# Optimization experiments

Measured on AMD Instinct MI355X. Metric: run time of the kernel, lower is better.

The kernel has to match this reference:

```python
import jax, jax.numpy as jnp
import numpy as np

N = 50000   # nodes
E = 400000  # directed edges (line-graph nodes)
LE = 1600000  # line-graph edges
B = 256     # graphs in batch
F = 64      # n_feats
ED = 16     # edge_dim
NIT = 3     # n_iter
SF = 6 * F  # LinearBlock hidden


def _seg_softmax(vals, seg, num):
    # numerically stable segment softmax (PyG softmax)
    m = jax.ops.segment_max(vals, seg, num_segments=num)
    e = jnp.exp(vals - m[seg])
    s = jax.ops.segment_sum(e, seg, num_segments=num)
    return e / (s[seg] + 1e-16)


def _gat_pool(out, lg_src, lg_dst, batch, gat_W, att_src, att_dst, gat_bias):
    # PyG GATConv(F, 1): heads=1, add_self_loops=True, negative_slope=0.2
    xw = out @ gat_W                       # [E, 1]
    sl = jnp.arange(E, dtype=lg_src.dtype)
    src = jnp.concatenate([lg_src, sl])
    dst = jnp.concatenate([lg_dst, sl])
    a_s = xw[:, 0] * att_src[0]
    a_d = xw[:, 0] * att_dst[0]
    alpha = jax.nn.leaky_relu(a_s[src] + a_d[dst], negative_slope=0.2)
    coef = _seg_softmax(alpha, dst, E)     # softmax over incoming line-edges
    xc = jax.ops.segment_sum(coef[:, None] * xw[src], dst, num_segments=E) + gat_bias  # [E,1]
    # GlobalAttentionPool: segment softmax over batch, then weighted sum pool
    sc = _seg_softmax(xc[:, 0], batch, B)[:, None]
    return jax.ops.segment_sum(out * sc, batch, num_segments=B)  # [B, F]


def _bn(x, g, b):
    # BatchNorm1d in training mode (batch stats, biased var, eps=1e-5)
    m = x.mean(0)
    v = ((x - m) ** 2).mean(0)
    return (x - m) * jax.lax.rsqrt(v + 1e-5) * g + b


def _prelu(x, w):
    return jnp.where(x >= 0, x, w * x)


def _lin_block(x, bn1_g, bn1_b, W1, b1, bn_g, bn_b, pr, W, b, bn5_g, bn5_b, pr5, W5, b5):
    x = _bn(x, bn1_g, bn1_b) @ W1 + b1                       # lin1: [N, 6F]
    h = _prelu(_bn(x, bn_g[0], bn_b[0]), pr[0]) @ W[0] + b[0]  # lin2
    h = _prelu(_bn(h, bn_g[1], bn_b[1]), pr[1]) @ W[1] + b[1]  # lin3
    x = (h + x) / 2
    x = (_prelu(_bn(x, bn_g[2], bn_b[2]), pr[2]) @ W[2] + b[2] + x) / 2  # lin4
    x = _prelu(_bn(x, bn5_g, bn5_b), pr5) @ W5 + b5          # lin5: [N, F]
    return x


def setup_inputs() -> dict:
    key = jax.random.key(0)
    ks = jax.random.split(key, 20)
    def nrm(k, shape, s=0.1):
        return jax.random.normal(k, shape, jnp.float32) * s
    inp = {}
    inp["x"] = jax.random.normal(ks[0], (N, F), jnp.float32)
    inp["edge_attr"] = jax.random.normal(ks[1], (E, ED), jnp.float32)
    inp["edge_index"] = jax.random.randint(ks[2], (2, E), 0, N, jnp.int32)
    inp["line_graph_edge_index"] = jax.random.randint(ks[3], (2, LE), 0, E, jnp.int32)
    inp["edge_index_batch"] = jnp.sort(jax.random.randint(ks[4], (E,), 0, B, jnp.int32))
    inp["W_u"] = nrm(ks[5], (F, F)); inp["W_v"] = nrm(ks[6], (F, F)); inp["W_e"] = nrm(ks[7], (ED, F))
    inp["gat_W"] = nrm(ks[8], (F, 1)); inp["gat_att_src"] = nrm(ks[9], (1,)); inp["gat_att_dst"] = nrm(ks[10], (1,))
    inp["gat_bias"] = jnp.zeros((1,), jnp.float32)
    inp["a"] = nrm(ks[11], (1, F, NIT)); inp["a_bias"] = jnp.zeros((1, 1, NIT), jnp.float32)
    inp["W_gout"] = nrm(ks[12], (F, F)); inp["b_gout"] = jnp.zeros((F,), jnp.float32)
    inp["lb_bn1_g"] = jnp.ones((F,), jnp.float32); inp["lb_bn1_b"] = jnp.zeros((F,), jnp.float32)
    inp["lb_W1"] = nrm(ks[13], (F, SF)); inp["lb_b1"] = jnp.zeros((SF,), jnp.float32)
    inp["lb_bn_g"] = jnp.ones((3, SF), jnp.float32); inp["lb_bn_b"] = jnp.zeros((3, SF), jnp.float32)
    inp["lb_pr"] = jnp.full((3,), 0.25, jnp.float32)
    inp["lb_W"] = nrm(ks[14], (3, SF, SF)); inp["lb_b"] = jnp.zeros((3, SF), jnp.float32)
    inp["lb_bn5_g"] = jnp.ones((SF,), jnp.float32); inp["lb_bn5_b"] = jnp.zeros((SF,), jnp.float32)
    inp["lb_pr5"] = jnp.array(0.25, jnp.float32)
    inp["lb_W5"] = nrm(ks[15], (SF, F)); inp["lb_b5"] = jnp.zeros((F,), jnp.float32)
    return inp


def reference(x, edge_attr, W_u, W_v, W_e, gat_W, gat_att_src, gat_att_dst, gat_bias,
              a, a_bias, W_gout, b_gout,
              lb_bn1_g, lb_bn1_b, lb_W1, lb_b1, lb_bn_g, lb_bn_b, lb_pr, lb_W, lb_b,
              lb_bn5_g, lb_bn5_b, lb_pr5, lb_W5, lb_b5,
              edge_index, line_graph_edge_index, edge_index_batch):
    ei0, ei1 = edge_index[0], edge_index[1]
    lg0, lg1 = line_graph_edge_index[0], line_graph_edge_index[1]
    # initial directed-edge features
    ea = ((x @ W_u)[ei0] + (x @ W_v)[ei1] + edge_attr @ W_e) / 3.0  # [E, F]
    out = ea
    outs, gouts = [], []
    for _ in range(NIT):
        out = ea + jax.ops.segment_sum(out[lg0], lg1, num_segments=E)  # line-graph message passing
        gout = _gat_pool(out, lg0, lg1, edge_index_batch, gat_W, gat_att_src, gat_att_dst, gat_bias)
        outs.append(out)
        gouts.append(jnp.tanh(gout @ W_gout + b_gout))
    out_all = jnp.stack(outs, -1)    # [E, F, NIT]
    gout_all = jnp.stack(gouts, -1)  # [B, F, NIT]
    sc = jax.nn.softmax((gout_all * a).sum(1, keepdims=True) + a_bias, axis=-1)  # [B,1,NIT]
    out = (out_all * sc[edge_index_batch]).sum(-1)  # per-edge gather == repeat_interleave(degree)
    xn = x + jax.ops.segment_sum(out, ei1, num_segments=N)
    return _lin_block(xn, lb_bn1_g, lb_bn1_b, lb_W1, lb_b1, lb_bn_g, lb_bn_b, lb_pr, lb_W, lb_b,
                      lb_bn5_g, lb_bn5_b, lb_pr5, lb_W5, lb_b5)
```

## Files before the change

### kernel.cpp

```cpp
#include <hip/hip_runtime.h>
#include <math.h>

#define NN 50000
#define EE 400000
#define LEE 1600000
#define BBATCH 256
#define FF 64
#define EDD 16
#define NITER 3
#define SFD 384

#define CDIV(a,b) (((a)+(b)-1)/(b))

typedef unsigned short ushort_t;
typedef __attribute__((ext_vector_type(8))) short bf16x8;
typedef __attribute__((ext_vector_type(4))) float f32x4;

__device__ inline float b2f(ushort_t u) { return __uint_as_float(((unsigned)u) << 16); }
__device__ inline ushort_t f2b(float f) {
    unsigned u = __float_as_uint(f);
    return (ushort_t)((u + 0x7fffu + ((u >> 16) & 1u)) >> 16);
}

__global__ void k_hist(const int* __restrict__ idx, int n, int* __restrict__ cnt) {
    int i = blockIdx.x * blockDim.x + threadIdx.x;
    if (i < n) atomicAdd(&cnt[idx[i]], 1);
}
__global__ void k_part(const int* __restrict__ in, int n, int* __restrict__ part) {
    __shared__ int s[256];
    int i = blockIdx.x * 256 + threadIdx.x;
    s[threadIdx.x] = (i < n) ? in[i] : 0;
    __syncthreads();
    for (int off = 128; off > 0; off >>= 1) {
        if (threadIdx.x < off) s[threadIdx.x] += s[threadIdx.x + off];
        __syncthreads();
    }
    if (threadIdx.x == 0) part[blockIdx.x] = s[0];
}
__global__ void k_scan_single(int* __restrict__ a, int n) {
    __shared__ int s[256];
    int v = (threadIdx.x < n) ? a[threadIdx.x] : 0;
    s[threadIdx.x] = v; __syncthreads();
    for (int off = 1; off < 256; off <<= 1) {
        int t = (threadIdx.x >= off) ? s[threadIdx.x - off] : 0;
        __syncthreads(); s[threadIdx.x] += t; __syncthreads();
    }
    if (threadIdx.x < n) a[threadIdx.x] = s[threadIdx.x] - v;
}
__global__ void k_scan_add(int* __restrict__ a, int n, const int* __restrict__ off) {
    __shared__ int s[256];
    int i = blockIdx.x * 256 + threadIdx.x;
    int v = (i < n) ? a[i] : 0;
    s[threadIdx.x] = v; __syncthreads();
    for (int o = 1; o < 256; o <<= 1) {
        int t = (threadIdx.x >= o) ? s[threadIdx.x - o] : 0;
        __syncthreads(); s[threadIdx.x] += t; __syncthreads();
    }
    if (i < n) a[i] = s[threadIdx.x] - v + off[blockIdx.x];
}
__global__ void k_scan_out(const int* __restrict__ in, int n, const int* __restrict__ boff,
                           int* __restrict__ out) {
    __shared__ int s[256];
    int i = blockIdx.x * 256 + threadIdx.x;
    int v = (i < n) ? in[i] : 0;
    s[threadIdx.x] = v; __syncthreads();
    for (int o = 1; o < 256; o <<= 1) {
        int t = (threadIdx.x >= o) ? s[threadIdx.x - o] : 0;
        __syncthreads(); s[threadIdx.x] += t; __syncthreads();
    }
    if (i < n) out[i] = s[threadIdx.x] - v + boff[blockIdx.x];
    if (i == n - 1) out[n] = s[threadIdx.x] + boff[blockIdx.x];
}
__global__ void k_fill_lg(const int* __restrict__ lg, const int* __restrict__ rowptr,
                          int* __restrict__ cnt, int* __restrict__ srcidx) {
    int i = blockIdx.x * blockDim.x + threadIdx.x;
    if (i >= LEE) return;
    int d = lg[LEE + i];
    int pos = rowptr[d] + atomicAdd(&cnt[d], 1);
    srcidx[pos] = lg[i];
}
__global__ void k_fill_n(const int* __restrict__ ei, const int* __restrict__ rowptr,
                         int* __restrict__ cnt, int* __restrict__ nidx) {
    int i = blockIdx.x * blockDim.x + threadIdx.x;
    if (i >= EE) return;
    int d = ei[EE + i];
    int pos = rowptr[d] + atomicAdd(&cnt[d], 1);
    nidx[pos] = i;
}


__global__ void k_node_mm(const float* __restrict__ x, const float* __restrict__ Wu,
                          const float* __restrict__ Wv, ushort_t* __restrict__ xu,
                          ushort_t* __restrict__ xv) {
    __shared__ float su[64 * 64];
    __shared__ float sv[64 * 64];
    int tid = threadIdx.x;
    for (int i = tid; i < 64 * 64; i += blockDim.x) { su[i] = Wu[i]; sv[i] = Wv[i]; }
    __syncthreads();
    int row = blockIdx.x * 4 + (tid >> 6);
    int f = tid & 63;
    if (row >= NN) return;
    const float* xr = x + (long long)row * 64;
    float au = 0.f, av = 0.f;
    #pragma unroll
    for (int k = 0; k < 64; ++k) {
        float xv_ = xr[k];
        au += xv_ * su[k * 64 + f];
        av += xv_ * sv[k * 64 + f];
    }
    xu[(long long)row * 64 + f] = f2b(au);
    xv[(long long)row * 64 + f] = f2b(av);
}

__global__ void k_ea_b16(const ushort_t* __restrict__ xu, const ushort_t* __restrict__ xv,
                         const float* __restrict__ eattr, const float* __restrict__ We,
                         const int* __restrict__ ei, ushort_t* __restrict__ eab) {
    __shared__ float swe[16 * 64];
    int tid = threadIdx.x;
    for (int i = tid; i < 1024; i += 256) swe[i] = We[i];
    __syncthreads();
    int e = blockIdx.x * 8 + (tid >> 5);
    int f2 = (tid & 31) * 2;
    if (e >= EE) return;
    int s = ei[e];
    int d = ei[EE + e];
    unsigned us = *(const unsigned*)&xu[(long long)s * 64 + f2];
    unsigned ud = *(const unsigned*)&xv[(long long)d * 64 + f2];
    const float* ar = eattr + (long long)e * 16;
    float a0 = 0.f, a1 = 0.f;
    #pragma unroll
    for (int k = 0; k < 16; ++k) {
        float w = ar[k];
        a0 += w * swe[k * 64 + f2];
        a1 += w * swe[k * 64 + f2 + 1];
    }
    float v0 = (b2f((ushort_t)us) + b2f((ushort_t)ud) + a0) * (1.0f / 3.0f);
    float v1 = (b2f((ushort_t)(us >> 16)) + b2f((ushort_t)(ud >> 16)) + a1) * (1.0f / 3.0f);
    *(unsigned*)&eab[(long long)e * 64 + f2] = (unsigned)f2b(v0) | ((unsigned)f2b(v1) << 16);
}

__global__ void k_mp_gather(const ushort_t* __restrict__ prev,
                            const ushort_t* __restrict__ eab,
                            const int* __restrict__ rowptr, const int* __restrict__ srcidx,
                            const float* __restrict__ gatW,
                            ushort_t* __restrict__ outb, float* __restrict__ xw) {
    int tid = threadIdx.x;
    int d = blockIdx.x * 8 + (tid >> 5);
    int f2 = (tid & 31) * 2;
    if (d >= EE) return;
    unsigned ue = *(const unsigned*)&eab[(long long)d * 64 + f2];
    float a0 = b2f((ushort_t)ue), a1 = b2f((ushort_t)(ue >> 16));
    int p0 = rowptr[d], p1 = rowptr[d + 1];
    int j = p0;
    for (; j + 4 <= p1; j += 4) {
        int s0 = srcidx[j], s1 = srcidx[j + 1], s2 = srcidx[j + 2], s3 = srcidx[j + 3];
        unsigned u0 = *(const unsigned*)&prev[(long long)s0 * 64 + f2];
        unsigned u1 = *(const unsigned*)&prev[(long long)s1 * 64 + f2];
        unsigned u2 = *(const unsigned*)&prev[(long long)s2 * 64 + f2];
        unsigned u3 = *(const unsigned*)&prev[(long long)s3 * 64 + f2];
        a0 += (b2f((ushort_t)u0) + b2f((ushort_t)u1)) + (b2f((ushort_t)u2) + b2f((ushort_t)u3));
        a1 += (b2f((ushort_t)(u0 >> 16)) + b2f((ushort_t)(u1 >> 16))) +
              (b2f((ushort_t)(u2 >> 16)) + b2f((ushort_t)(u3 >> 16)));
    }
    for (; j < p1; ++j) {
        unsigned u0 = *(const unsigned*)&prev[(long long)srcidx[j] * 64 + f2];
        a0 += b2f((ushort_t)u0);
        a1 += b2f((ushort_t)(u0 >> 16));
    }
    *(unsigned*)&outb[(long long)d * 64 + f2] = (unsigned)f2b(a0) | ((unsigned)f2b(a1) << 16);
    float w = a0 * gatW[f2] + a1 * gatW[f2 + 1];
    #pragma unroll
    for (int o = 16; o > 0; o >>= 1) w += __shfl_down(w, o, 32);
    if ((tid & 31) == 0) xw[d] = w;
}

__global__ void k_gat_fused(const float* __restrict__ xw,
                            const int* __restrict__ rowptr, const int* __restrict__ srcidx,
                            const float* __restrict__ att_s, const float* __restrict__ att_d,
                            const float* __restrict__ gbias, float* __restrict__ xc) {
    int e = blockIdx.x * blockDim.x + threadIdx.x;
    if (e >= EE) return;
    float as = att_s[0], ad = att_d[0];
    float xwd = xw[e];
    float adt = xwd * ad;
    float aself = xwd * as + adt;
    if (aself < 0.f) aself *= 0.2f;
    float m = aself;
    float ssum = 1.0f;
    float wsum = xwd;
    int p0 = rowptr[e], p1 = rowptr[e + 1];
    for (int j = p0; j < p1; ++j) {
        float xs = xw[srcidx[j]];
        float a = xs * as + adt;
        if (a < 0.f) a *= 0.2f;
        if (a > m) {
            float r = expf(m - a);
            ssum = ssum * r + 1.0f;
            wsum = wsum * r + xs;
            m = a;
        } else {
            float ev = expf(a - m);
            ssum += ev;
            wsum += ev * xs;
        }
    }
    xc[e] = wsum / (ssum + 1e-16f) + gbias[0];
}

__global__ void k_batchptr(const int* __restrict__ batch, int* __restrict__ bptr) {
    int e = blockIdx.x * blockDim.x + threadIdx.x;
    if (e >= EE) return;
    int b = batch[e];
    int bp = (e == 0) ? -1 : batch[e - 1];
    for (int q = bp + 1; q <= b; ++q) bptr[q] = e;
    if (e == EE - 1)
        for (int q = b + 1; q <= BBATCH; ++q) bptr[q] = EE;
}

__global__ void k_pool(const float* __restrict__ xc, const ushort_t* __restrict__ out,
                       const int* __restrict__ bptr, float* __restrict__ gout) {
    int b = blockIdx.x;
    int p0 = bptr[b], p1 = bptr[b + 1];
    __shared__ float red[256];
    int tid = threadIdx.x;
    float mx = -INFINITY;
    for (int e = p0 + tid; e < p1; e += 256) mx = fmaxf(mx, xc[e]);
    red[tid] = mx; __syncthreads();
    for (int s = 128; s > 0; s >>= 1) { if (tid < s) red[tid] = fmaxf(red[tid], red[tid + s]); __syncthreads(); }
    float m = red[0]; __syncthreads();
    float sm = 0.f;
    for (int e = p0 + tid; e < p1; e += 256) sm += expf(xc[e] - m);
    red[tid] = sm; __syncthreads();
    for (int s = 128; s > 0; s >>= 1) { if (tid < s) red[tid] += red[tid + s]; __syncthreads(); }
    float ssum = red[0] + 1e-16f; __syncthreads();
    int f = tid & 63, chunk = tid >> 6;
    float acc = 0.f;
    for (int e = p0 + chunk; e < p1; e += 4) {
        float w = expf(xc[e] - m);
        acc += w * b2f(out[(long long)e * 64 + f]);
    }
    red[tid] = acc; __syncthreads();
    if (chunk == 0) {
        float tot = red[f] + red[64 + f] + red[128 + f] + red[192 + f];
        gout[b * 64 + f] = tot / ssum;
    }
}

__global__ void k_gout_mm(const float* __restrict__ gout, const float* __restrict__ Wg,
                          const float* __restrict__ bg, float* __restrict__ gt) {
    __shared__ float sw[64 * 64];
    int tid = threadIdx.x;
    for (int i = tid; i < 4096; i += blockDim.x) sw[i] = Wg[i];
    __syncthreads();
    int row = blockIdx.x * 4 + (tid >> 6);
    int f = tid & 63;
    if (row >= BBATCH) return;
    const float* gr = gout + row * 64;
    float acc = bg[f];
    #pragma unroll
    for (int k = 0; k < 64; ++k) acc += gr[k] * sw[k * 64 + f];
    gt[row * 64 + f] = tanhf(acc);
}

__global__ void k_att(const float* __restrict__ g0, const float* __restrict__ g1,
                      const float* __restrict__ g2, const float* __restrict__ a,
                      const float* __restrict__ abias, float* __restrict__ sc) {
    int b = blockIdx.x;
    int f = threadIdx.x;
    float v0 = g0[b * 64 + f] * a[f * 3 + 0];
    float v1 = g1[b * 64 + f] * a[f * 3 + 1];
    float v2 = g2[b * 64 + f] * a[f * 3 + 2];
    #pragma unroll
    for (int o = 32; o > 0; o >>= 1) {
        v0 += __shfl_down(v0, o, 64);
        v1 += __shfl_down(v1, o, 64);
        v2 += __shfl_down(v2, o, 64);
    }
    if (f == 0) {
        float s0 = v0 + abias[0], s1 = v1 + abias[1], s2 = v2 + abias[2];
        float m = fmaxf(s0, fmaxf(s1, s2));
        float e0 = expf(s0 - m), e1 = expf(s1 - m), e2 = expf(s2 - m);
        float inv = 1.0f / (e0 + e1 + e2);
        sc[b * 3 + 0] = e0 * inv; sc[b * 3 + 1] = e1 * inv; sc[b * 3 + 2] = e2 * inv;
    }
}

__global__ void k_comb(ushort_t* __restrict__ o1, const ushort_t* __restrict__ o2,
                       const ushort_t* __restrict__ o3, const float* __restrict__ sc,
                       const int* __restrict__ batch) {
    long long idx = (long long)blockIdx.x * blockDim.x + threadIdx.x;
    if (idx >= (long long)EE * 64) return;
    int e = (int)(idx >> 6);
    int b = batch[e];
    float v = b2f(o1[idx]) * sc[b * 3] + b2f(o2[idx]) * sc[b * 3 + 1] + b2f(o3[idx]) * sc[b * 3 + 2];
    o1[idx] = f2b(v);
}

__global__ void k_node_gather(const ushort_t* __restrict__ comb, const int* __restrict__ nrow,
                              const int* __restrict__ nidx, const float* __restrict__ x,
                              ushort_t* __restrict__ xnb) {
    int tid = threadIdx.x;
    int n = blockIdx.x * 4 + (tid >> 6);
    int f = tid & 63;
    if (n >= NN) return;
    float acc = x[(long long)n * 64 + f];
    int p0 = nrow[n], p1 = nrow[n + 1];
    int j = p0;
    for (; j + 4 <= p1; j += 4) {
        int e0 = nidx[j], e1 = nidx[j + 1], e2 = nidx[j + 2], e3 = nidx[j + 3];
        float v0 = b2f(comb[(long long)e0 * 64 + f]);
        float v1 = b2f(comb[(long long)e1 * 64 + f]);
        float v2 = b2f(comb[(long long)e2 * 64 + f]);
        float v3 = b2f(comb[(long long)e3 * 64 + f]);
        acc += (v0 + v1) + (v2 + v3);
    }
    for (; j < p1; ++j) acc += b2f(comb[(long long)nidx[j] * 64 + f]);
    xnb[(long long)n * 64 + f] = f2b(acc);
}

__global__ void k_colstats_b16(const ushort_t* __restrict__ X, int ncols, int nrows,
                               float* __restrict__ csum, float* __restrict__ csumsq) {
    int c = threadIdx.x;
    int rpb = CDIV(nrows, (int)gridDim.x);
    int r0 = blockIdx.x * rpb;
    int r1 = min(r0 + rpb, nrows);
    float s = 0.f, s2 = 0.f;
    for (int r = r0; r < r1; ++r) {
        float v = b2f(X[(long long)r * ncols + c]);
        s += v; s2 += v * v;
    }
    atomicAdd(&csum[c], s);
    atomicAdd(&csumsq[c], s2);
}

__global__ void k_wtrans(const float* __restrict__ W, int K, int M, ushort_t* __restrict__ Wt) {
    __shared__ ushort_t tile[32][33];
    int kb = blockIdx.y * 32, mb = blockIdx.x * 32;
    int tx = threadIdx.x & 31, ty = threadIdx.x >> 5;
    for (int dy = ty; dy < 32; dy += 8) {
        int k = kb + dy, m = mb + tx;
        tile[dy][tx] = (k < K && m < M) ? f2b(W[(long long)k * M + m]) : (ushort_t)0;
    }
    __syncthreads();
    for (int dy = ty; dy < 32; dy += 8) {
        int m = mb + dy, k = kb + tx;
        if (m < M && k < K) Wt[(long long)m * K + k] = tile[tx][dy];
    }
}

template<int KK, int MT, int WR, int WC, int RT>
__global__ __launch_bounds__(512) void k_gemm_fused(
    const ushort_t* __restrict__ A, const ushort_t* __restrict__ Wt,
    const float* __restrict__ bias, const ushort_t* __restrict__ resb,
    const float* __restrict__ csum, const float* __restrict__ csumsq,
    const float* __restrict__ g, const float* __restrict__ bb,
    const float* __restrict__ pr, float scale, int nrows,
    ushort_t* __restrict__ Cb, float* __restrict__ Cf,
    float* __restrict__ osum, float* __restrict__ osumsq) {
    constexpr int RTW = RT / WR;
    constexpr int MTW = MT / WC;
    constexpr int FM = RTW / 16;
    constexpr int FN = MTW / 16;
    __shared__ ushort_t sA[RT][36];
    __shared__ float sScl[KK], sOff[KK];
    __shared__ float sStatS[MT], sStatQ[MT];
    int tid = threadIdx.x;
    int wave = tid >> 6, lane = tid & 63;
    int l16 = lane & 15, klo = lane >> 4;
    int wrow = wave / WC, wcol = wave % WC;
    long long rowBase = (long long)blockIdx.x * RT;
    float prs = pr ? pr[0] : 1.0f;
    const float invn = 1.0f / (float)NN;
    for (int c = tid; c < KK; c += 512) {
        float mean = csum[c] * invn;
        float var = csumsq[c] * invn - mean * mean;
        float scl = rsqrtf(var + 1e-5f) * g[c];
        sScl[c] = scl;
        sOff[c] = bb[c] - mean * scl;
    }
    if (osum) {
        for (int c = tid; c < MT; c += 512) { sStatS[c] = 0.f; sStatQ[c] = 0.f; }
    }
    __syncthreads();
    f32x4 acc[FM][FN] = {};
    for (int k0 = 0; k0 < KK; k0 += 32) {
        #pragma unroll
        for (int it = 0; it < RT * 32 / (512 * 8); ++it) {
            int idx = (it * 512 + tid) * 8;
            int r = idx >> 5, kk = idx & 31;
            long long gr = rowBase + r;
            uint4 raw = {0u, 0u, 0u, 0u};
            if (gr < nrows) raw = *(const uint4*)&A[gr * KK + k0 + kk];
            unsigned outw[4];
            #pragma unroll
            for (int q = 0; q < 4; ++q) {
                unsigned rw = ((const unsigned*)&raw)[q];
                int c = k0 + kk + q * 2;
                float t0 = b2f((ushort_t)rw) * sScl[c] + sOff[c];
                float t1 = b2f((ushort_t)(rw >> 16)) * sScl[c + 1] + sOff[c + 1];
                if (t0 < 0.f) t0 *= prs;
                if (t1 < 0.f) t1 *= prs;
                outw[q] = (unsigned)f2b(t0) | ((unsigned)f2b(t1) << 16);
            }
            uint2 w0; w0.x = outw[0]; w0.y = outw[1];
            uint2 w1; w1.x = outw[2]; w1.y = outw[3];
            *(uint2*)&sA[r][kk] = w0;
            *(uint2*)&sA[r][kk + 4] = w1;
        }
        __syncthreads();
        bf16x8 bfr[FN];
        #pragma unroll
        for (int n = 0; n < FN; ++n) {
            int col = wcol * MTW + n * 16 + l16;
            bfr[n] = *(const bf16x8*)&Wt[(long long)col * KK + k0 + klo * 8];
        }
        bf16x8 afr[FM];
        #pragma unroll
        for (int m = 0; m < FM; ++m) {
            union { uint2 p[2]; bf16x8 v; } u;
            int row = wrow * RTW + m * 16 + l16;
            u.p[0] = *(const uint2*)&sA[row][klo * 8];
            u.p[1] = *(const uint2*)&sA[row][klo * 8 + 4];
            afr[m] = u.v;
        }
        #pragma unroll
        for (int m = 0; m < FM; ++m)
            #pragma unroll
            for (int n = 0; n < FN; ++n)
                acc[m][n] = __builtin_amdgcn_mfma_f32_16x16x32_bf16(afr[m], bfr[n], acc[m][n], 0, 0, 0);
        __syncthreads();
    }
    #pragma unroll
    for (int m = 0; m < FM; ++m) {
        #pragma unroll
        for (int n = 0; n < FN; ++n) {
            int col = wcol * MTW + n * 16 + l16;
            long long row0 = rowBase + wrow * RTW + m * 16 + klo * 4;
            float bcol = bias[col];
            float s = 0.f, s2 = 0.f;
            #pragma unroll
            for (int r = 0; r < 4; ++r) {
                long long row = row0 + r;
                if (row < nrows) {
                    float v = acc[m][n][r] + bcol;
                    if (resb) v += b2f(resb[row * MT + col]);
                    v *= scale;
                    if (Cf) Cf[row * MT + col] = v;
                    if (Cb) Cb[row * MT + col] = f2b(v);
                    s += v; s2 += v * v;
                }
            }
            if (osum) {
                s += __shfl_down(s, 32, 64);
                s2 += __shfl_down(s2, 32, 64);
                s += __shfl_down(s, 16, 64);
                s2 += __shfl_down(s2, 16, 64);
                if (lane < 16) {
                    atomicAdd(&sStatS[col], s);
                    atomicAdd(&sStatQ[col], s2);
                }
            }
        }
    }
    if (osum) {
        __syncthreads();
        for (int c = tid; c < MT; c += 512) {
            atomicAdd(&osum[c], sStatS[c]);
            atomicAdd(&osumsq[c], sStatQ[c]);
        }
    }
}

extern "C" void kernel_launch(void* const* d_in, const int* in_sizes, int n_in,
                              void* d_out, int out_size, void* d_ws, size_t ws_size,
                              hipStream_t stream) {
    const float* x       = (const float*)d_in[0];
    const float* eattr   = (const float*)d_in[1];
    const int*   ei      = (const int*)d_in[2];
    const int*   lg      = (const int*)d_in[3];
    const int*   batch   = (const int*)d_in[4];
    const float* W_u     = (const float*)d_in[5];
    const float* W_v     = (const float*)d_in[6];
    const float* W_e     = (const float*)d_in[7];
    const float* gat_W   = (const float*)d_in[8];
    const float* att_s   = (const float*)d_in[9];
    const float* att_d   = (const float*)d_in[10];
    const float* gat_b   = (const float*)d_in[11];
    const float* a_att   = (const float*)d_in[12];
    const float* a_bias  = (const float*)d_in[13];
    const float* W_gout  = (const float*)d_in[14];
    const float* b_gout  = (const float*)d_in[15];
    const float* bn1_g   = (const float*)d_in[16];
    const float* bn1_b   = (const float*)d_in[17];
    const float* lb_W1   = (const float*)d_in[18];
    const float* lb_b1   = (const float*)d_in[19];
    const float* lb_bn_g = (const float*)d_in[20];
    const float* lb_bn_b = (const float*)d_in[21];
    const float* lb_pr   = (const float*)d_in[22];
    const float* lb_W    = (const float*)d_in[23];
    const float* lb_b    = (const float*)d_in[24];
    const float* bn5_g   = (const float*)d_in[25];
    const float* bn5_b   = (const float*)d_in[26];
    const float* pr5     = (const float*)d_in[27];
    const float* lb_W5   = (const float*)d_in[28];
    const float* lb_b5   = (const float*)d_in[29];
    float* out_final = (float*)d_out;

    const long long ESZ = (long long)EE * FF;
    const long long NSZ = (long long)NN * FF;
    char* cur = (char*)d_ws;
    auto alloc = [&](size_t bytes) -> void* {
        void* p = (void*)cur;
        cur += (bytes + 255) & ~(size_t)255;
        return p;
    };
    ushort_t* XU = (ushort_t*)alloc(NSZ * 2);
    ushort_t* XV = (ushort_t*)alloc(NSZ * 2);
    ushort_t* O1 = (ushort_t*)alloc(ESZ * 2);
    ushort_t* O2 = (ushort_t*)alloc(ESZ * 2);
    ushort_t* O3 = (ushort_t*)alloc(ESZ * 2);
    float* XW = (float*)alloc((size_t)EE * 4);
    float* XC = (float*)alloc((size_t)EE * 4);
    ushort_t* XNB = (ushort_t*)alloc(NSZ * 2);
    float* GRAW = (float*)alloc(BBATCH * FF * 4);
    float* G0 = (float*)alloc(BBATCH * FF * 4);
    float* G1 = (float*)alloc(BBATCH * FF * 4);
    float* G2 = (float*)alloc(BBATCH * FF * 4);
    float* SCATT = (float*)alloc(BBATCH * 3 * 4);
    int* BPTR = (int*)alloc((BBATCH + 1) * 4);
    int* LROW = (int*)alloc((size_t)(EE + 1) * 4);
    int* LSRC = (int*)alloc((size_t)LEE * 4);
    int* LCNT = (int*)alloc((size_t)EE * 4);
    int* NROW = (int*)alloc((size_t)(NN + 1) * 4);
    int* NIDX = (int*)alloc((size_t)EE * 4);
    int* NCNT = (int*)alloc((size_t)NN * 4);
    int* SP0 = (int*)alloc(2048 * 4);
    int* SP1 = (int*)alloc(256 * 4);
    float* STATS = (float*)alloc(5 * 2 * SFD * 4);
    ushort_t* WT1 = (ushort_t*)alloc((size_t)SFD * FF * 2);
    ushort_t* WT2 = (ushort_t*)alloc((size_t)SFD * SFD * 2);
    ushort_t* WT3 = (ushort_t*)alloc((size_t)SFD * SFD * 2);
    ushort_t* WT4 = (ushort_t*)alloc((size_t)SFD * SFD * 2);
    ushort_t* WT5 = (ushort_t*)alloc((size_t)FF * SFD * 2);
    if ((size_t)(cur - (char*)d_ws) > ws_size) return;

    ushort_t* T1B = O1;
    ushort_t* T2B = T1B + (long long)NN * SFD;
    ushort_t* T3B = T2B + (long long)NN * SFD;
    ushort_t* T4B = T3B + (long long)NN * SFD;
    float* CS[5][2];
    for (int i = 0; i < 5; ++i) { CS[i][0] = STATS + i * 2 * SFD; CS[i][1] = CS[i][0] + SFD; }
    float* GTS[3] = {G0, G1, G2};

    hipMemsetAsync(STATS, 0, 5 * 2 * SFD * 4, stream);

    {
        dim3 gt(SFD / 32, FF / 32);
        k_wtrans<<<gt, 256, 0, stream>>>(lb_W1, FF, SFD, WT1);
        dim3 gs(SFD / 32, SFD / 32);
        k_wtrans<<<gs, 256, 0, stream>>>(lb_W, SFD, SFD, WT2);
        k_wtrans<<<gs, 256, 0, stream>>>(lb_W + (long long)SFD * SFD, SFD, SFD, WT3);
        k_wtrans<<<gs, 256, 0, stream>>>(lb_W + 2LL * SFD * SFD, SFD, SFD, WT4);
        dim3 g5(FF / 32, SFD / 32);
        k_wtrans<<<g5, 256, 0, stream>>>(lb_W5, SFD, FF, WT5);
    }

    k_node_mm<<<CDIV(NN, 4), 256, 0, stream>>>(x, W_u, W_v, XU, XV);
    k_batchptr<<<CDIV(EE, 256), 256, 0, stream>>>(batch, BPTR);

    {
        hipMemsetAsync(LCNT, 0, (size_t)EE * 4, stream);
        k_hist<<<CDIV(LEE, 256), 256, 0, stream>>>(lg + LEE, LEE, LCNT);
        int nb0 = CDIV(EE, 256), nb1 = CDIV(nb0, 256);
        k_part<<<nb0, 256, 0, stream>>>(LCNT, EE, SP0);
        k_part<<<nb1, 256, 0, stream>>>(SP0, nb0, SP1);
        k_scan_single<<<1, 256, 0, stream>>>(SP1, nb1);
        k_scan_add<<<nb1, 256, 0, stream>>>(SP0, nb0, SP1);
        k_scan_out<<<nb0, 256, 0, stream>>>(LCNT, EE, SP0, LROW);
        hipMemsetAsync(LCNT, 0, (size_t)EE * 4, stream);
        k_fill_lg<<<CDIV(LEE, 256), 256, 0, stream>>>(lg, LROW, LCNT, LSRC);
    }
    {
        hipMemsetAsync(NCNT, 0, (size_t)NN * 4, stream);
        k_hist<<<CDIV(EE, 256), 256, 0, stream>>>(ei + EE, EE, NCNT);
        int nb0 = CDIV(NN, 256), nb1 = CDIV(nb0, 256);
        k_part<<<nb0, 256, 0, stream>>>(NCNT, NN, SP0);
        k_part<<<nb1, 256, 0, stream>>>(SP0, nb0, SP1);
        k_scan_single<<<1, 256, 0, stream>>>(SP1, nb1);
        k_scan_add<<<nb1, 256, 0, stream>>>(SP0, nb0, SP1);
        k_scan_out<<<nb0, 256, 0, stream>>>(NCNT, NN, SP0, NROW);
        hipMemsetAsync(NCNT, 0, (size_t)NN * 4, stream);
        k_fill_n<<<CDIV(EE, 256), 256, 0, stream>>>(ei, NROW, NCNT, NIDX);
    }

    const int EB8 = CDIV(EE, 8);

    auto gat_pool = [&](ushort_t* buf, int t) {
        k_gat_fused<<<CDIV(EE, 256), 256, 0, stream>>>(XW, LROW, LSRC, att_s, att_d, gat_b, XC);
        k_pool<<<BBATCH, 256, 0, stream>>>(XC, buf, BPTR, GRAW);
        k_gout_mm<<<CDIV(BBATCH, 4), 256, 0, stream>>>(GRAW, W_gout, b_gout, GTS[t]);
    };

    k_ea_b16<<<EB8, 256, 0, stream>>>(XU, XV, eattr, W_e, ei, O3);
    k_mp_gather<<<EB8, 256, 0, stream>>>(O3, O3, LROW, LSRC, gat_W, O1, XW);
    gat_pool(O1, 0);
    k_mp_gather<<<EB8, 256, 0, stream>>>(O1, O3, LROW, LSRC, gat_W, O2, XW);
    gat_pool(O2, 1);
    k_mp_gather<<<EB8, 256, 0, stream>>>(O2, O3, LROW, LSRC, gat_W, O3, XW);
    gat_pool(O3, 2);

    k_att<<<BBATCH, 64, 0, stream>>>(G0, G1, G2, a_att, a_bias, SCATT);
    k_comb<<<(int)CDIV(ESZ, 256), 256, 0, stream>>>(O1, O2, O3, SCATT, batch);
    k_node_gather<<<CDIV(NN, 4), 256, 0, stream>>>(O1, NROW, NIDX, x, XNB);
    k_colstats_b16<<<256, FF, 0, stream>>>(XNB, FF, NN, CS[0][0], CS[0][1]);

    {
        const int GB128 = CDIV(NN, 128);
        k_gemm_fused<64, 384, 2, 4, 128><<<GB128, 512, 0, stream>>>(XNB, WT1, lb_b1, nullptr,
            CS[0][0], CS[0][1], bn1_g, bn1_b, nullptr, 1.0f, NN,
            T1B, nullptr, CS[1][0], CS[1][1]);
        k_gemm_fused<384, 384, 2, 4, 128><<<GB128, 512, 0, stream>>>(T1B, WT2, lb_b, nullptr,
            CS[1][0], CS[1][1], lb_bn_g, lb_bn_b, lb_pr, 1.0f, NN,
            T2B, nullptr, CS[2][0], CS[2][1]);
        k_gemm_fused<384, 384, 2, 4, 128><<<GB128, 512, 0, stream>>>(T2B, WT3, lb_b + SFD, T1B,
            CS[2][0], CS[2][1], lb_bn_g + SFD, lb_bn_b + SFD, lb_pr + 1, 0.5f, NN,
            T3B, nullptr, CS[3][0], CS[3][1]);
        k_gemm_fused<384, 384, 2, 4, 128><<<GB128, 512, 0, stream>>>(T3B, WT4, lb_b + 2 * SFD, T3B,
            CS[3][0], CS[3][1], lb_bn_g + 2 * SFD, lb_bn_b + 2 * SFD, lb_pr + 2, 0.5f, NN,
            T4B, nullptr, CS[4][0], CS[4][1]);
        k_gemm_fused<384, 64, 8, 1, 256><<<CDIV(NN, 256), 512, 0, stream>>>(T4B, WT5, lb_b5, nullptr,
            CS[4][0], CS[4][1], bn5_g, bn5_b, pr5, 1.0f, NN,
            nullptr, out_final, nullptr, nullptr);
    }
}
```

Before: 1.793 ms.

## Split BN+PReLU into separate pass and stage GEMM A tiles via global_load_lds

After: 1.855 ms. +3.5%, slower.

```diff
diff --git a/kernel.cpp b/kernel.cpp
--- a/kernel.cpp
+++ b/kernel.cpp
@@ -15,6 +15,10 @@
 typedef unsigned short ushort_t;
 typedef __attribute__((ext_vector_type(8))) short bf16x8;
 typedef __attribute__((ext_vector_type(4))) float f32x4;
+
+#define GLOAD_LDS16(gp, lp) __builtin_amdgcn_global_load_lds( \
+    (const __attribute__((address_space(1))) void*)(gp), \
+    (__attribute__((address_space(3))) void*)(lp), 16, 0, 0)
 
 __device__ inline float b2f(ushort_t u) { return __uint_as_float(((unsigned)u) << 16); }
 __device__ inline ushort_t f2b(float f) {
@@ -348,86 +352,99 @@
     }
 }
 
+__global__ void k_bnact(const ushort_t* __restrict__ X, const float* __restrict__ csum,
+                        const float* __restrict__ csumsq, const float* __restrict__ g,
+                        const float* __restrict__ bb, const float* __restrict__ pr,
+                        int ncols, long long nvec, ushort_t* __restrict__ Y) {
+    __shared__ float sScl[SFD], sOff[SFD];
+    const float invn = 1.0f / (float)NN;
+    for (int c = threadIdx.x; c < ncols; c += blockDim.x) {
+        float mean = csum[c] * invn;
+        float var = csumsq[c] * invn - mean * mean;
+        float scl = rsqrtf(var + 1e-5f) * g[c];
+        sScl[c] = scl;
+        sOff[c] = bb[c] - mean * scl;
+    }
+    __syncthreads();
+    float prs = pr ? pr[0] : 1.0f;
+    long long i = (long long)blockIdx.x * blockDim.x + threadIdx.x;
+    if (i >= nvec) return;
+    uint4 raw = ((const uint4*)X)[i];
+    int cb = (int)(((unsigned long long)i * 8) % (unsigned)ncols);
+    unsigned outw[4];
+    #pragma unroll
+    for (int q = 0; q < 4; ++q) {
+        unsigned rw = ((const unsigned*)&raw)[q];
+        int c = cb + q * 2;
+        float t0 = b2f((ushort_t)rw) * sScl[c] + sOff[c];
+        float t1 = b2f((ushort_t)(rw >> 16)) * sScl[c + 1] + sOff[c + 1];
+        if (t0 < 0.f) t0 *= prs;
+        if (t1 < 0.f) t1 *= prs;
+        outw[q] = (unsigned)f2b(t0) | ((unsigned)f2b(t1) << 16);
+    }
+    uint4 o; o.x = outw[0]; o.y = outw[1]; o.z = outw[2]; o.w = outw[3];
+    ((uint4*)Y)[i] = o;
+}
+
 template<int KK, int MT, int WR, int WC, int RT>
-__global__ __launch_bounds__(512) void k_gemm_fused(
+__global__ __launch_bounds__(512) void k_gemm2(
     const ushort_t* __restrict__ A, const ushort_t* __restrict__ Wt,
     const float* __restrict__ bias, const ushort_t* __restrict__ resb,
-    const float* __restrict__ csum, const float* __restrict__ csumsq,
-    const float* __restrict__ g, const float* __restrict__ bb,
-    const float* __restrict__ pr, float scale, int nrows,
+    float scale, int nrows,
     ushort_t* __restrict__ Cb, float* __restrict__ Cf,
     float* __restrict__ osum, float* __restrict__ osumsq) {
+    constexpr int BK = 64;
     constexpr int RTW = RT / WR;
     constexpr int MTW = MT / WC;
     constexpr int FM = RTW / 16;
     constexpr int FN = MTW / 16;
-    __shared__ ushort_t sA[RT][36];
-    __shared__ float sScl[KK], sOff[KK];
+    constexpr int CALLS = RT * BK * 2 / (512 * 16);
+    __shared__ ushort_t sA[RT][BK];
     __shared__ float sStatS[MT], sStatQ[MT];
     int tid = threadIdx.x;
     int wave = tid >> 6, lane = tid & 63;
     int l16 = lane & 15, klo = lane >> 4;
     int wrow = wave / WC, wcol = wave % WC;
     long long rowBase = (long long)blockIdx.x * RT;
-    float prs = pr ? pr[0] : 1.0f;
-    const float invn = 1.0f / (float)NN;
-    for (int c = tid; c < KK; c += 512) {
-        float mean = csum[c] * invn;
-        float var = csumsq[c] * invn - mean * mean;
-        float scl = rsqrtf(var + 1e-5f) * g[c];
-        sScl[c] = scl;
-        sOff[c] = bb[c] - mean * scl;
-    }
     if (osum) {
         for (int c = tid; c < MT; c += 512) { sStatS[c] = 0.f; sStatQ[c] = 0.f; }
     }
-    __syncthreads();
     f32x4 acc[FM][FN] = {};
-    for (int k0 = 0; k0 < KK; k0 += 32) {
+    for (int s = 0; s < KK / BK; ++s) {
+        int k0 = s * BK;
         #pragma unroll
-        for (int it = 0; it < RT * 32 / (512 * 8); ++it) {
-            int idx = (it * 512 + tid) * 8;
-            int r = idx >> 5, kk = idx & 31;
-            long long gr = rowBase + r;
-            uint4 raw = {0u, 0u, 0u, 0u};
-            if (gr < nrows) raw = *(const uint4*)&A[gr * KK + k0 + kk];
-            unsigned outw[4];
-            #pragma unroll
-            for (int q = 0; q < 4; ++q) {
-                unsigned rw = ((const unsigned*)&raw)[q];
-                int c = k0 + kk + q * 2;
-                float t0 = b2f((ushort_t)rw) * sScl[c] + sOff[c];
-                float t1 = b2f((ushort_t)(rw >> 16)) * sScl[c + 1] + sOff[c + 1];
-                if (t0 < 0.f) t0 *= prs;
-                if (t1 < 0.f) t1 *= prs;
-                outw[q] = (unsigned)f2b(t0) | ((unsigned)f2b(t1) << 16);
-            }
-            uint2 w0; w0.x = outw[0]; w0.y = outw[1];
-            uint2 w1; w1.x = outw[2]; w1.y = outw[3];
-            *(uint2*)&sA[r][kk] = w0;
-            *(uint2*)&sA[r][kk + 4] = w1;
+        for (int c = 0; c < CALLS; ++c) {
+            int lin = c * 512 + tid;
+            int row = lin >> 3;
+            int wb = (lin & 7) * 16;
+            int swb = wb ^ ((row & 7) << 4);
+            long long gr = rowBase + row;
+            const ushort_t* gp = &A[gr * KK + k0] + (swb >> 1);
+            ushort_t* lp = &sA[0][0] + (long long)(c * 512 + wave * 64) * 8;
+            if (gr < nrows) GLOAD_LDS16(gp, lp);
         }
         __syncthreads();
-        bf16x8 bfr[FN];
         #pragma unroll
-        for (int n = 0; n < FN; ++n) {
-            int col = wcol * MTW + n * 16 + l16;
-            bfr[n] = *(const bf16x8*)&Wt[(long long)col * KK + k0 + klo * 8];
+        for (int kk = 0; kk < BK; kk += 32) {
+            bf16x8 bfr[FN];
+            #pragma unroll
+            for (int n = 0; n < FN; ++n) {
+                int col = wcol * MTW + n * 16 + l16;
+                bfr[n] = *(const bf16x8*)&Wt[(long long)col * KK + k0 + kk + klo * 8];
+            }
+            bf16x8 afr[FM];
+            #pragma unroll
+            for (int m = 0; m < FM; ++m) {
+                int row = wrow * RTW + m * 16 + l16;
+                int fb = (kk + klo * 8) * 2;
+                afr[m] = *(const bf16x8*)((const char*)&sA[0][0] + row * 128 + (fb ^ ((row & 7) << 4)));
+            }
+            #pragma unroll
+            for (int m = 0; m < FM; ++m)
+                #pragma unroll
+                for (int n = 0; n < FN; ++n)
+                    acc[m][n] = __builtin_amdgcn_mfma_f32_16x16x32_bf16(afr[m], bfr[n], acc[m][n], 0, 0, 0);
         }
-        bf16x8 afr[FM];
-        #pragma unroll
-        for (int m = 0; m < FM; ++m) {
-            union { uint2 p[2]; bf16x8 v; } u;
-            int row = wrow * RTW + m * 16 + l16;
-            u.p[0] = *(const uint2*)&sA[row][klo * 8];
-            u.p[1] = *(const uint2*)&sA[row][klo * 8 + 4];
-            afr[m] = u.v;
-        }
-        #pragma unroll
-        for (int m = 0; m < FM; ++m)
-            #pragma unroll
-            for (int n = 0; n < FN; ++n)
-                acc[m][n] = __builtin_amdgcn_mfma_f32_16x16x32_bf16(afr[m], bfr[n], acc[m][n], 0, 0, 0);
         __syncthreads();
     }
     #pragma unroll
@@ -508,6 +525,7 @@
 
     const long long ESZ = (long long)EE * FF;
     const long long NSZ = (long long)NN * FF;
+    const long long NSF = (long long)NN * SFD;
     char* cur = (char*)d_ws;
     auto alloc = [&](size_t bytes) -> void* {
         void* p = (void*)cur;
@@ -542,12 +560,13 @@
     ushort_t* WT3 = (ushort_t*)alloc((size_t)SFD * SFD * 2);
     ushort_t* WT4 = (ushort_t*)alloc((size_t)SFD * SFD * 2);
     ushort_t* WT5 = (ushort_t*)alloc((size_t)FF * SFD * 2);
+    ushort_t* ACT = (ushort_t*)alloc((size_t)NSF * 2);
     if ((size_t)(cur - (char*)d_ws) > ws_size) return;
 
     ushort_t* T1B = O1;
-    ushort_t* T2B = T1B + (long long)NN * SFD;
-    ushort_t* T3B = T2B + (long long)NN * SFD;
-    ushort_t* T4B = T3B + (long long)NN * SFD;
+    ushort_t* T2B = T1B + NSF;
+    ushort_t* T3B = T2B + NSF;
+    ushort_t* T4B = T3B + NSF;
     float* CS[5][2];
     for (int i = 0; i < 5; ++i) { CS[i][0] = STATS + i * 2 * SFD; CS[i][1] = CS[i][0] + SFD; }
     float* GTS[3] = {G0, G1, G2};
@@ -616,20 +635,26 @@
 
     {
         const int GB128 = CDIV(NN, 128);
-        k_gemm_fused<64, 384, 2, 4, 128><<<GB128, 512, 0, stream>>>(XNB, WT1, lb_b1, nullptr,
-            CS[0][0], CS[0][1], bn1_g, bn1_b, nullptr, 1.0f, NN,
-            T1B, nullptr, CS[1][0], CS[1][1]);
-        k_gemm_fused<384, 384, 2, 4, 128><<<GB128, 512, 0, stream>>>(T1B, WT2, lb_b, nullptr,
-            CS[1][0], CS[1][1], lb_bn_g, lb_bn_b, lb_pr, 1.0f, NN,
-            T2B, nullptr, CS[2][0], CS[2][1]);
-        k_gemm_fused<384, 384, 2, 4, 128><<<GB128, 512, 0, stream>>>(T2B, WT3, lb_b + SFD, T1B,
-            CS[2][0], CS[2][1], lb_bn_g + SFD, lb_bn_b + SFD, lb_pr + 1, 0.5f, NN,
-            T3B, nullptr, CS[3][0], CS[3][1]);
-        k_gemm_fused<384, 384, 2, 4, 128><<<GB128, 512, 0, stream>>>(T3B, WT4, lb_b + 2 * SFD, T3B,
-            CS[3][0], CS[3][1], lb_bn_g + 2 * SFD, lb_bn_b + 2 * SFD, lb_pr + 2, 0.5f, NN,
-            T4B, nullptr, CS[4][0], CS[4][1]);
-        k_gemm_fused<384, 64, 8, 1, 256><<<CDIV(NN, 256), 512, 0, stream>>>(T4B, WT5, lb_b5, nullptr,
-            CS[4][0], CS[4][1], bn5_g, bn5_b, pr5, 1.0f, NN,
-            nullptr, out_final, nullptr, nullptr);
-    }
-}
+        const long long NV64 = NSZ / 8, NV384 = NSF / 8;
+        k_bnact<<<(int)CDIV(NV64, 256), 256, 0, stream>>>(XNB, CS[0][0], CS[0][1],
+            bn1_g, bn1_b, nullptr, FF, NV64, ACT);
+        k_gemm2<64, 384, 2, 4, 128><<<GB128, 512, 0, stream>>>(ACT, WT1, lb_b1, nullptr,
+            1.0f, NN, T1B, nullptr, CS[1][0], CS[1][1]);
+        k_bnact<<<(int)CDIV(NV384, 256), 256, 0, stream>>>(T1B, CS[1][0], CS[1][1],
+            lb_bn_g, lb_bn_b, lb_pr, SFD, NV384, ACT);
+        k_gemm2<384, 384, 2, 4, 128><<<GB128, 512, 0, stream>>>(ACT, WT2, lb_b, nullptr,
+            1.0f, NN, T2B, nullptr, CS[2][0], CS[2][1]);
+        k_bnact<<<(int)CDIV(NV384, 256), 256, 0, stream>>>(T2B, CS[2][0], CS[2][1],
+            lb_bn_g + SFD, lb_bn_b + SFD, lb_pr + 1, SFD, NV384, ACT);
+        k_gemm2<384, 384, 2, 4, 128><<<GB128, 512, 0, stream>>>(ACT, WT3, lb_b + SFD, T1B,
+            0.5f, NN, T3B, nullptr, CS[3][0], CS[3][1]);
+        k_bnact<<<(int)CDIV(NV384, 256), 256, 0, stream>>>(T3B, CS[3][0], CS[3][1],
+            lb_bn_g + 2 * SFD, lb_bn_b + 2 * SFD, lb_pr + 2, SFD, NV384, ACT);
+        k_gemm2<384, 384, 2, 4, 128><<<GB128, 512, 0, stream>>>(ACT, WT4, lb_b + 2 * SFD, T3B,
+            0.5f, NN, T4B, nullptr, CS[4][0], CS[4][1]);
+        k_bnact<<<(int)CDIV(NV384, 256), 256, 0, stream>>>(T4B, CS[4][0], CS[4][1],
+            bn5_g, bn5_b, pr5, SFD, NV384, ACT);
+        k_gemm2<384, 64, 8, 1, 256><<<CDIV(NN, 256), 512, 0, stream>>>(ACT, WT5, lb_b5, nullptr,
+            1.0f, NN, nullptr, out_final, nullptr, nullptr);
+    }
+}
```
